# Kernel tuning notes

Hardware: AMD Instinct MI355X
Metric: run time of the kernel (lower is better)

## Reference

```python
import jax, jax.numpy as jnp
import numpy as np

B, T, E, H = 2, 1024, 1024, 16
HD = E // H
TEMP = 0.5


def setup_inputs() -> dict:
    key = jax.random.key(0)
    ks = jax.random.split(key, 20)
    d = {
        "query1": jax.random.normal(ks[0], (B, T, E), jnp.float32),
        "query2": jax.random.normal(ks[1], (B, T, E), jnp.float32),
        "key": jax.random.normal(ks[2], (B, T, E), jnp.float32),
        "value": jax.random.normal(ks[3], (B, T, E), jnp.float32),
    }
    s = 1.0 / np.sqrt(E)
    names = ["Wq", "Wq2", "Wq3", "Wk", "Wv", "Wo"]
    for i, n in enumerate(names):
        d[n] = jax.random.normal(ks[4 + i], (E, E), jnp.float32) * s
        d["b" + n[1:]] = jax.random.normal(ks[10 + i], (E,), jnp.float32) * 0.01
    return d


def _heads(x):
    # [B,T,E] -> [B,H,T,HD]
    b, t, _ = x.shape
    return x.reshape(b, t, H, HD).transpose(0, 2, 1, 3)


def reference(query1, query2, key, value,
              Wq, bq, Wq2, bq2, Wq3, bq3, Wk, bk, Wv, bv, Wo, bo):
    q = _heads(query1 @ Wq.T + bq)
    q2 = _heads(query2 @ Wq2.T + bq2)
    q3 = _heads(key @ Wq3.T + bq3)
    k = _heads(key @ Wk.T + bk)
    v = _heads(value @ Wv.T + bv)
    b, _, t, _ = q.shape
    scale = 1.0 / np.sqrt(HD)

    def global_attn(qx):
        s = jnp.einsum('bhtd,bhsd->bhts', qx, k) * scale  # [B,H,T,T]
        # global softmax over flattened T*T, temperature-scaled, times T
        a = jax.nn.softmax((s / TEMP).reshape(b, H, t * t), axis=-1)
        return a.reshape(b, H, t, t) * t

    a1 = global_attn(q)
    a2 = global_attn(q2)
    a3 = global_attn(q3)
    attn_out = jnp.einsum('bhts,bhsd->bthd', (a1 + a2 + a3) / 3.0, v)
    attn_out = attn_out.reshape(b, t, E)
    output = attn_out @ Wo.T + bo
    return output, a1
```

## Files before the change

kernel.cpp:

```cpp
#include <hip/hip_runtime.h>
#include <hip/hip_bf16.h>


#define B_ 2
#define T_ 1024
#define E_ 1024
#define H_ 16
#define HD_ 64
#define BH_ 32

typedef float f32x4 __attribute__((ext_vector_type(4)));
typedef short bfrag __attribute__((ext_vector_type(8)));

__device__ __forceinline__ unsigned short f2b(float f) {
  unsigned int u = __float_as_uint(f);
  u += 0x7fffu + ((u >> 16) & 1u);
  return (unsigned short)(u >> 16);
}

struct CvtArgs { const float* src[10]; unsigned short* dst[10]; int n[10]; };

__global__ __launch_bounds__(256) void cvt_kernel(CvtArgs a) {
  const int z = blockIdx.y;
  const float* __restrict__ s = a.src[z];
  unsigned short* __restrict__ d = a.dst[z];
  const int n = a.n[z];
  const int stride = gridDim.x * 256 * 4;
  for (int i = (blockIdx.x * 256 + threadIdx.x) * 4; i < n; i += stride) {
    float4 v = *(const float4*)(s + i);
    ushort4 o;
    o.x = f2b(v.x); o.y = f2b(v.y); o.z = f2b(v.z); o.w = f2b(v.w);
    *(ushort4*)(d + i) = o;
  }
}

__device__ __forceinline__ void mm128_core(const unsigned short* __restrict__ A,
                                           const unsigned short* __restrict__ W,
                                           int m0, int n0,
                                           unsigned short* As, unsigned short* Bs,
                                           f32x4 acc[4][4]) {
  const int tid  = threadIdx.x;
  const int lane = tid & 63, w = tid >> 6;
  const int lrow = lane & 15, quad = lane >> 4;
  const int wm = (w >> 1) * 64, wn = (w & 1) * 64;
  const int srow = tid >> 2, soff = (tid & 3) * 8;

  const unsigned short* Ar0 = A + (size_t)(m0 + srow) * E_ + soff;
  const unsigned short* Ar1 = Ar0 + (size_t)64 * E_;
  const unsigned short* Br0 = W + (size_t)(n0 + srow) * E_ + soff;
  const unsigned short* Br1 = Br0 + (size_t)64 * E_;

  for (int k0 = 0; k0 < E_; k0 += 32) {
    int4 a0 = *(const int4*)(Ar0 + k0);
    int4 a1 = *(const int4*)(Ar1 + k0);
    int4 b0 = *(const int4*)(Br0 + k0);
    int4 b1 = *(const int4*)(Br1 + k0);
    __syncthreads();
    *(int4*)(As + srow * 32 + soff)        = a0;
    *(int4*)(As + (srow + 64) * 32 + soff) = a1;
    *(int4*)(Bs + srow * 32 + soff)        = b0;
    *(int4*)(Bs + (srow + 64) * 32 + soff) = b1;
    __syncthreads();
    bfrag af[4], bf_[4];
#pragma unroll
    for (int mt = 0; mt < 4; mt++)
      af[mt] = *(const bfrag*)(As + (wm + mt * 16 + lrow) * 32 + quad * 8);
#pragma unroll
    for (int nt = 0; nt < 4; nt++)
      bf_[nt] = *(const bfrag*)(Bs + (wn + nt * 16 + lrow) * 32 + quad * 8);
#pragma unroll
    for (int mt = 0; mt < 4; mt++)
#pragma unroll
      for (int nt = 0; nt < 4; nt++)
        acc[mt][nt] = __builtin_amdgcn_mfma_f32_16x16x32_bf16(af[mt], bf_[nt], acc[mt][nt], 0, 0, 0);
  }
}

struct ProjArgs {
  const unsigned short* X[5];
  const unsigned short* W[5];
  const float* bias[5];
  unsigned short* dst[5];
};

__global__ __launch_bounds__(256) void proj_kernel(ProjArgs pa) {
  __shared__ unsigned short As[128 * 32];
  __shared__ unsigned short Bs[128 * 32];
  const int z = blockIdx.z;
  const int m0 = blockIdx.y * 128, n0 = blockIdx.x * 128;
  f32x4 acc[4][4];
#pragma unroll
  for (int mt = 0; mt < 4; mt++)
#pragma unroll
    for (int nt = 0; nt < 4; nt++) acc[mt][nt] = (f32x4)0.f;

  mm128_core(pa.X[z], pa.W[z], m0, n0, As, Bs, acc);

  const int tid = threadIdx.x, lane = tid & 63, w = tid >> 6;
  const int lrow = lane & 15, quad = lane >> 4;
  const int wm = (w >> 1) * 64, wn = (w & 1) * 64;
  const float* __restrict__ bias = pa.bias[z];
  unsigned short* __restrict__ dst = pa.dst[z];
  float bv[4];
#pragma unroll
  for (int nt = 0; nt < 4; nt++) bv[nt] = bias[n0 + wn + nt * 16 + lrow];
#pragma unroll
  for (int mt = 0; mt < 4; mt++)
#pragma unroll
    for (int nt = 0; nt < 4; nt++)
#pragma unroll
      for (int ii = 0; ii < 4; ii++) {
        const int m = m0 + wm + mt * 16 + quad * 4 + ii;
        const int n = n0 + wn + nt * 16 + lrow;
        const float v = acc[mt][nt][ii] + bv[nt];
        const int b = m >> 10, t = m & 1023, h = n >> 6, dd = n & 63;
        size_t idx;
        if (z == 4)
          idx = ((size_t)((b * H_ + h) * HD_ + dd)) * T_ + t;
        else
          idx = ((size_t)((b * H_ + h) * T_ + t)) * HD_ + dd;
        dst[idx] = f2b(v);
      }
}

__global__ __launch_bounds__(256) void attn_sums_kernel(
    const unsigned short* __restrict__ Q1, const unsigned short* __restrict__ Q2,
    const unsigned short* __restrict__ Q3, const unsigned short* __restrict__ Kh,
    float* __restrict__ sums) {
  const int tid = threadIdx.x, lane = tid & 63, w = tid >> 6;
  const int lrow = lane & 15, quad = lane >> 4;
  const int tw = w >> 1, sw = w & 1;
  const int bh = blockIdx.y;
  const int tb = blockIdx.x * 128 + tw * 64;
  const size_t base = (size_t)bh * T_ * HD_;
  const unsigned short* Qs[3] = {Q1 + base, Q2 + base, Q3 + base};
  const unsigned short* Kb = Kh + base;

  float lsum[3] = {0.f, 0.f, 0.f};
  for (int s0 = 0; s0 < T_; s0 += 128) {
    const int sb = s0 + sw * 64;
#pragma unroll
    for (int i = 0; i < 3; i++) {
      f32x4 acc[4][4];
#pragma unroll
      for (int mt = 0; mt < 4; mt++)
#pragma unroll
        for (int nt = 0; nt < 4; nt++) acc[mt][nt] = (f32x4)0.f;
#pragma unroll
      for (int kk = 0; kk < 2; kk++) {
        bfrag af[4], bf_[4];
#pragma unroll
        for (int mt = 0; mt < 4; mt++)
          af[mt] = *(const bfrag*)(Qs[i] + (size_t)(tb + mt * 16 + lrow) * HD_ + kk * 32 + quad * 8);
#pragma unroll
        for (int nt = 0; nt < 4; nt++)
          bf_[nt] = *(const bfrag*)(Kb + (size_t)(sb + nt * 16 + lrow) * HD_ + kk * 32 + quad * 8);
#pragma unroll
        for (int mt = 0; mt < 4; mt++)
#pragma unroll
          for (int nt = 0; nt < 4; nt++)
            acc[mt][nt] = __builtin_amdgcn_mfma_f32_16x16x32_bf16(af[mt], bf_[nt], acc[mt][nt], 0, 0, 0);
      }
      float s = 0.f;
#pragma unroll
      for (int mt = 0; mt < 4; mt++)
#pragma unroll
        for (int nt = 0; nt < 4; nt++)
#pragma unroll
          for (int ii = 0; ii < 4; ii++)
            s += __expf(acc[mt][nt][ii] * 0.25f);
      lsum[i] += s;
    }
  }
#pragma unroll
  for (int i = 0; i < 3; i++) {
    float v = lsum[i];
    for (int off = 32; off > 0; off >>= 1) v += __shfl_down(v, off, 64);
    if (lane == 0) atomicAdd(&sums[i * BH_ + bh], v);
  }
}

__global__ __launch_bounds__(256) void attn_main_kernel(
    const unsigned short* __restrict__ Q1, const unsigned short* __restrict__ Q2,
    const unsigned short* __restrict__ Q3, const unsigned short* __restrict__ Kh,
    const unsigned short* __restrict__ Vt, const float* __restrict__ sums,
    float* __restrict__ a1out, unsigned short* __restrict__ attn_out) {
  __shared__ unsigned short P[128 * 136];
  const int tid = threadIdx.x, lane = tid & 63, w = tid >> 6;
  const int lrow = lane & 15, quad = lane >> 4;
  const int tw = w >> 1, sw = w & 1, dw = sw;
  const int bh = blockIdx.y;
  const int b = bh >> 4, h = bh & 15;
  const int tb = blockIdx.x * 128 + tw * 64;
  const size_t base = (size_t)bh * T_ * HD_;
  const unsigned short* Qs[3] = {Q1 + base, Q2 + base, Q3 + base};
  const unsigned short* Kb = Kh + base;
  const unsigned short* Vb = Vt + (size_t)bh * HD_ * T_;

  float r[3];
#pragma unroll
  for (int i = 0; i < 3; i++) r[i] = (float)T_ / (3.f * sums[i * BH_ + bh]);
  const float a1s = 3.f * r[0];

  f32x4 oacc[4][2];
#pragma unroll
  for (int mt = 0; mt < 4; mt++) { oacc[mt][0] = (f32x4)0.f; oacc[mt][1] = (f32x4)0.f; }

  for (int s0 = 0; s0 < T_; s0 += 128) {
    const int sb = s0 + sw * 64;
    f32x4 pc[4][4];
#pragma unroll
    for (int mt = 0; mt < 4; mt++)
#pragma unroll
      for (int nt = 0; nt < 4; nt++) pc[mt][nt] = (f32x4)0.f;

#pragma unroll
    for (int i = 0; i < 3; i++) {
      f32x4 acc[4][4];
#pragma unroll
      for (int mt = 0; mt < 4; mt++)
#pragma unroll
        for (int nt = 0; nt < 4; nt++) acc[mt][nt] = (f32x4)0.f;
#pragma unroll
      for (int kk = 0; kk < 2; kk++) {
        bfrag af[4], bf_[4];
#pragma unroll
        for (int mt = 0; mt < 4; mt++)
          af[mt] = *(const bfrag*)(Qs[i] + (size_t)(tb + mt * 16 + lrow) * HD_ + kk * 32 + quad * 8);
#pragma unroll
        for (int nt = 0; nt < 4; nt++)
          bf_[nt] = *(const bfrag*)(Kb + (size_t)(sb + nt * 16 + lrow) * HD_ + kk * 32 + quad * 8);
#pragma unroll
        for (int mt = 0; mt < 4; mt++)
#pragma unroll
          for (int nt = 0; nt < 4; nt++)
            acc[mt][nt] = __builtin_amdgcn_mfma_f32_16x16x32_bf16(af[mt], bf_[nt], acc[mt][nt], 0, 0, 0);
      }
      const float ri = r[i];
#pragma unroll
      for (int mt = 0; mt < 4; mt++)
#pragma unroll
        for (int nt = 0; nt < 4; nt++)
#pragma unroll
          for (int ii = 0; ii < 4; ii++) {
            const float e = __expf(acc[mt][nt][ii] * 0.25f);
            pc[mt][nt][ii] += ri * e;
            if (i == 0) {
              const int t = tb + mt * 16 + quad * 4 + ii;
              const int s = sb + nt * 16 + lrow;
              a1out[((size_t)bh * T_ + t) * T_ + s] = e * a1s;
            }
          }
    }
    __syncthreads();
#pragma unroll
    for (int mt = 0; mt < 4; mt++)
#pragma unroll
      for (int nt = 0; nt < 4; nt++)
#pragma unroll
        for (int ii = 0; ii < 4; ii++) {
          const int tl = tw * 64 + mt * 16 + quad * 4 + ii;
          const int sl = sw * 64 + nt * 16 + lrow;
          P[tl * 136 + sl] = f2b(pc[mt][nt][ii]);
        }
    __syncthreads();
#pragma unroll
    for (int kk = 0; kk < 4; kk++) {
      bfrag pf[4], vf[2];
#pragma unroll
      for (int mt = 0; mt < 4; mt++)
        pf[mt] = *(const bfrag*)(P + (tw * 64 + mt * 16 + lrow) * 136 + kk * 32 + quad * 8);
#pragma unroll
      for (int nt = 0; nt < 2; nt++)
        vf[nt] = *(const bfrag*)(Vb + (size_t)(dw * 32 + nt * 16 + lrow) * T_ + s0 + kk * 32 + quad * 8);
#pragma unroll
      for (int mt = 0; mt < 4; mt++)
#pragma unroll
        for (int nt = 0; nt < 2; nt++)
          oacc[mt][nt] = __builtin_amdgcn_mfma_f32_16x16x32_bf16(pf[mt], vf[nt], oacc[mt][nt], 0, 0, 0);
    }
  }
#pragma unroll
  for (int mt = 0; mt < 4; mt++)
#pragma unroll
    for (int nt = 0; nt < 2; nt++)
#pragma unroll
      for (int ii = 0; ii < 4; ii++) {
        const int t = tb + mt * 16 + quad * 4 + ii;
        const int dd = dw * 32 + nt * 16 + lrow;
        attn_out[((size_t)(b * T_ + t)) * E_ + h * HD_ + dd] = f2b(oacc[mt][nt][ii]);
      }
}

__global__ __launch_bounds__(256) void outproj_kernel(
    const unsigned short* __restrict__ Ab, const unsigned short* __restrict__ Wb,
    const float* __restrict__ bias, float* __restrict__ out) {
  __shared__ unsigned short As[128 * 32];
  __shared__ unsigned short Bs[128 * 32];
  const int m0 = blockIdx.y * 128, n0 = blockIdx.x * 128;
  f32x4 acc[4][4];
#pragma unroll
  for (int mt = 0; mt < 4; mt++)
#pragma unroll
    for (int nt = 0; nt < 4; nt++) acc[mt][nt] = (f32x4)0.f;

  mm128_core(Ab, Wb, m0, n0, As, Bs, acc);

  const int tid = threadIdx.x, lane = tid & 63, w = tid >> 6;
  const int lrow = lane & 15, quad = lane >> 4;
  const int wm = (w >> 1) * 64, wn = (w & 1) * 64;
  float bv[4];
#pragma unroll
  for (int nt = 0; nt < 4; nt++) bv[nt] = bias[n0 + wn + nt * 16 + lrow];
#pragma unroll
  for (int mt = 0; mt < 4; mt++)
#pragma unroll
    for (int nt = 0; nt < 4; nt++)
#pragma unroll
      for (int ii = 0; ii < 4; ii++) {
        const int m = m0 + wm + mt * 16 + quad * 4 + ii;
        const int n = n0 + wn + nt * 16 + lrow;
        out[(size_t)m * E_ + n] = acc[mt][nt][ii] + bv[nt];
      }
}

extern "C" void kernel_launch(void* const* d_in, const int* in_sizes, int n_in,
                              void* d_out, int out_size, void* d_ws, size_t ws_size,
                              hipStream_t stream) {
  const float* q1f  = (const float*)d_in[0];
  const float* q2f  = (const float*)d_in[1];
  const float* keyf = (const float*)d_in[2];
  const float* valf = (const float*)d_in[3];
  const float* Wq  = (const float*)d_in[4];  const float* bq  = (const float*)d_in[5];
  const float* Wq2 = (const float*)d_in[6];  const float* bq2 = (const float*)d_in[7];
  const float* Wq3 = (const float*)d_in[8];  const float* bq3 = (const float*)d_in[9];
  const float* Wk  = (const float*)d_in[10]; const float* bk  = (const float*)d_in[11];
  const float* Wv  = (const float*)d_in[12]; const float* bv  = (const float*)d_in[13];
  const float* Wo  = (const float*)d_in[14]; const float* bo  = (const float*)d_in[15];

  char* ws = (char*)d_ws;
  const size_t MB = 1024 * 1024;
  unsigned short* xq1  = (unsigned short*)(ws + 0 * MB);
  unsigned short* xq2  = (unsigned short*)(ws + 4 * MB);
  unsigned short* xkey = (unsigned short*)(ws + 8 * MB);
  unsigned short* xval = (unsigned short*)(ws + 12 * MB);
  unsigned short* wq   = (unsigned short*)(ws + 16 * MB);
  unsigned short* wq2  = (unsigned short*)(ws + 18 * MB);
  unsigned short* wq3  = (unsigned short*)(ws + 20 * MB);
  unsigned short* wk   = (unsigned short*)(ws + 22 * MB);
  unsigned short* wv   = (unsigned short*)(ws + 24 * MB);
  unsigned short* wo   = (unsigned short*)(ws + 26 * MB);
  unsigned short* Qh1  = (unsigned short*)(ws + 28 * MB);
  unsigned short* Qh2  = (unsigned short*)(ws + 32 * MB);
  unsigned short* Qh3  = (unsigned short*)(ws + 36 * MB);
  unsigned short* Kh   = (unsigned short*)(ws + 40 * MB);
  unsigned short* Vt   = (unsigned short*)(ws + 44 * MB);
  unsigned short* attn = (unsigned short*)(ws + 48 * MB);
  float* sums          = (float*)(ws + 52 * MB);

  CvtArgs ca;
  const float* srcs[10] = {q1f, q2f, keyf, valf, Wq, Wq2, Wq3, Wk, Wv, Wo};
  unsigned short* dsts[10] = {xq1, xq2, xkey, xval, wq, wq2, wq3, wk, wv, wo};
  for (int i = 0; i < 10; i++) { ca.src[i] = srcs[i]; ca.dst[i] = dsts[i]; ca.n[i] = (i < 4) ? 2097152 : 1048576; }
  cvt_kernel<<<dim3(2048, 10), 256, 0, stream>>>(ca);

  hipMemsetAsync(sums, 0, 3 * BH_ * sizeof(float), stream);

  ProjArgs pa;
  const unsigned short* Xs[5] = {xq1, xq2, xkey, xkey, xval};
  const unsigned short* Ws_[5] = {wq, wq2, wq3, wk, wv};
  const float* Bi[5] = {bq, bq2, bq3, bk, bv};
  unsigned short* Ds[5] = {Qh1, Qh2, Qh3, Kh, Vt};
  for (int i = 0; i < 5; i++) { pa.X[i] = Xs[i]; pa.W[i] = Ws_[i]; pa.bias[i] = Bi[i]; pa.dst[i] = Ds[i]; }
  proj_kernel<<<dim3(8, 16, 5), 256, 0, stream>>>(pa);

  attn_sums_kernel<<<dim3(8, BH_), 256, 0, stream>>>(Qh1, Qh2, Qh3, Kh, sums);

  float* out = (float*)d_out;
  attn_main_kernel<<<dim3(8, BH_), 256, 0, stream>>>(Qh1, Qh2, Qh3, Kh, Vt, sums,
                                                     out + 2097152, attn);

  outproj_kernel<<<dim3(8, 16), 256, 0, stream>>>(attn, wo, bo, out);
}
```

Before: 372.1 us.

## Shrink attention tiles for more blocks, use exp2 and direct global-to-LDS loads

```diff
diff --git a/kernel.cpp b/kernel.cpp
--- a/kernel.cpp
+++ b/kernel.cpp
@@ -9,6 +9,8 @@
 #define HD_ 64
 #define BH_ 32
 
+#define CEXP 0.36067376022224085f
+
 typedef float f32x4 __attribute__((ext_vector_type(4)));
 typedef short bfrag __attribute__((ext_vector_type(8)));
 
@@ -16,6 +18,15 @@
   unsigned int u = __float_as_uint(f);
   u += 0x7fffu + ((u >> 16) & 1u);
   return (unsigned short)(u >> 16);
+}
+
+__device__ __forceinline__ void gl_lds16(const unsigned short* g, unsigned short* l) {
+  __builtin_amdgcn_global_load_lds(
+      reinterpret_cast<const __attribute__((address_space(1))) unsigned int*>(
+          reinterpret_cast<uintptr_t>(g)),
+      reinterpret_cast<__attribute__((address_space(3))) unsigned int*>(
+          reinterpret_cast<uintptr_t>(l)),
+      16, 0, 0);
 }
 
 struct CvtArgs { const float* src[10]; unsigned short* dst[10]; int n[10]; };
@@ -49,17 +60,17 @@
   const unsigned short* Ar1 = Ar0 + (size_t)64 * E_;
   const unsigned short* Br0 = W + (size_t)(n0 + srow) * E_ + soff;
   const unsigned short* Br1 = Br0 + (size_t)64 * E_;
+  unsigned short* Ad0 = As + tid * 8;
+  unsigned short* Ad1 = As + 2048 + tid * 8;
+  unsigned short* Bd0 = Bs + tid * 8;
+  unsigned short* Bd1 = Bs + 2048 + tid * 8;
 
   for (int k0 = 0; k0 < E_; k0 += 32) {
-    int4 a0 = *(const int4*)(Ar0 + k0);
-    int4 a1 = *(const int4*)(Ar1 + k0);
-    int4 b0 = *(const int4*)(Br0 + k0);
-    int4 b1 = *(const int4*)(Br1 + k0);
     __syncthreads();
-    *(int4*)(As + srow * 32 + soff)        = a0;
-    *(int4*)(As + (srow + 64) * 32 + soff) = a1;
-    *(int4*)(Bs + srow * 32 + soff)        = b0;
-    *(int4*)(Bs + (srow + 64) * 32 + soff) = b1;
+    gl_lds16(Ar0 + k0, Ad0);
+    gl_lds16(Ar1 + k0, Ad1);
+    gl_lds16(Br0 + k0, Bd0);
+    gl_lds16(Br1 + k0, Bd1);
     __syncthreads();
     bfrag af[4], bf_[4];
 #pragma unroll
@@ -123,75 +134,79 @@
       }
 }
 
-__global__ __launch_bounds__(256) void attn_sums_kernel(
+__global__ __launch_bounds__(256, 4) void attn_sums_kernel(
     const unsigned short* __restrict__ Q1, const unsigned short* __restrict__ Q2,
     const unsigned short* __restrict__ Q3, const unsigned short* __restrict__ Kh,
     float* __restrict__ sums) {
   const int tid = threadIdx.x, lane = tid & 63, w = tid >> 6;
   const int lrow = lane & 15, quad = lane >> 4;
   const int tw = w >> 1, sw = w & 1;
-  const int bh = blockIdx.y;
-  const int tb = blockIdx.x * 128 + tw * 64;
+  const int bh = blockIdx.z;
+  const int tb = blockIdx.x * 64 + tw * 32;
+  const int sbase = blockIdx.y * 512;
   const size_t base = (size_t)bh * T_ * HD_;
   const unsigned short* Qs[3] = {Q1 + base, Q2 + base, Q3 + base};
   const unsigned short* Kb = Kh + base;
 
-  float lsum[3] = {0.f, 0.f, 0.f};
-  for (int s0 = 0; s0 < T_; s0 += 128) {
-    const int sb = s0 + sw * 64;
+  float ls[3][4];
+#pragma unroll
+  for (int i = 0; i < 3; i++)
+#pragma unroll
+    for (int ii = 0; ii < 4; ii++) ls[i][ii] = 0.f;
+
+  for (int j = 0; j < 4; j++) {
+    const int sb = sbase + j * 128 + sw * 64;
 #pragma unroll
     for (int i = 0; i < 3; i++) {
-      f32x4 acc[4][4];
-#pragma unroll
-      for (int mt = 0; mt < 4; mt++)
+      f32x4 acc[2][4];
+#pragma unroll
+      for (int mt = 0; mt < 2; mt++)
 #pragma unroll
         for (int nt = 0; nt < 4; nt++) acc[mt][nt] = (f32x4)0.f;
 #pragma unroll
       for (int kk = 0; kk < 2; kk++) {
-        bfrag af[4], bf_[4];
-#pragma unroll
-        for (int mt = 0; mt < 4; mt++)
+        bfrag af[2], bf_[4];
+#pragma unroll
+        for (int mt = 0; mt < 2; mt++)
           af[mt] = *(const bfrag*)(Qs[i] + (size_t)(tb + mt * 16 + lrow) * HD_ + kk * 32 + quad * 8);
 #pragma unroll
         for (int nt = 0; nt < 4; nt++)
           bf_[nt] = *(const bfrag*)(Kb + (size_t)(sb + nt * 16 + lrow) * HD_ + kk * 32 + quad * 8);
 #pragma unroll
-        for (int mt = 0; mt < 4; mt++)
+        for (int mt = 0; mt < 2; mt++)
 #pragma unroll
           for (int nt = 0; nt < 4; nt++)
             acc[mt][nt] = __builtin_amdgcn_mfma_f32_16x16x32_bf16(af[mt], bf_[nt], acc[mt][nt], 0, 0, 0);
       }
-      float s = 0.f;
-#pragma unroll
-      for (int mt = 0; mt < 4; mt++)
+#pragma unroll
+      for (int mt = 0; mt < 2; mt++)
 #pragma unroll
         for (int nt = 0; nt < 4; nt++)
 #pragma unroll
           for (int ii = 0; ii < 4; ii++)
-            s += __expf(acc[mt][nt][ii] * 0.25f);
-      lsum[i] += s;
+            ls[i][ii] += exp2f(acc[mt][nt][ii] * CEXP);
     }
   }
 #pragma unroll
   for (int i = 0; i < 3; i++) {
-    float v = lsum[i];
+    float v = (ls[i][0] + ls[i][1]) + (ls[i][2] + ls[i][3]);
     for (int off = 32; off > 0; off >>= 1) v += __shfl_down(v, off, 64);
     if (lane == 0) atomicAdd(&sums[i * BH_ + bh], v);
   }
 }
 
-__global__ __launch_bounds__(256) void attn_main_kernel(
+__global__ __launch_bounds__(256, 2) void attn_main_kernel(
     const unsigned short* __restrict__ Q1, const unsigned short* __restrict__ Q2,
     const unsigned short* __restrict__ Q3, const unsigned short* __restrict__ Kh,
     const unsigned short* __restrict__ Vt, const float* __restrict__ sums,
     float* __restrict__ a1out, unsigned short* __restrict__ attn_out) {
-  __shared__ unsigned short P[128 * 136];
+  __shared__ unsigned short P[64 * 136];
   const int tid = threadIdx.x, lane = tid & 63, w = tid >> 6;
   const int lrow = lane & 15, quad = lane >> 4;
   const int tw = w >> 1, sw = w & 1, dw = sw;
   const int bh = blockIdx.y;
   const int b = bh >> 4, h = bh & 15;
-  const int tb = blockIdx.x * 128 + tw * 64;
+  const int tb = blockIdx.x * 64 + tw * 32;
   const size_t base = (size_t)bh * T_ * HD_;
   const unsigned short* Qs[3] = {Q1 + base, Q2 + base, Q3 + base};
   const unsigned short* Kb = Kh + base;
@@ -202,48 +217,48 @@
   for (int i = 0; i < 3; i++) r[i] = (float)T_ / (3.f * sums[i * BH_ + bh]);
   const float a1s = 3.f * r[0];
 
-  f32x4 oacc[4][2];
-#pragma unroll
-  for (int mt = 0; mt < 4; mt++) { oacc[mt][0] = (f32x4)0.f; oacc[mt][1] = (f32x4)0.f; }
+  f32x4 oacc[2][2];
+#pragma unroll
+  for (int mt = 0; mt < 2; mt++) { oacc[mt][0] = (f32x4)0.f; oacc[mt][1] = (f32x4)0.f; }
 
   for (int s0 = 0; s0 < T_; s0 += 128) {
     const int sb = s0 + sw * 64;
-    f32x4 pc[4][4];
-#pragma unroll
-    for (int mt = 0; mt < 4; mt++)
+    f32x4 pc[2][4];
+#pragma unroll
+    for (int mt = 0; mt < 2; mt++)
 #pragma unroll
       for (int nt = 0; nt < 4; nt++) pc[mt][nt] = (f32x4)0.f;
 
 #pragma unroll
     for (int i = 0; i < 3; i++) {
-      f32x4 acc[4][4];
-#pragma unroll
-      for (int mt = 0; mt < 4; mt++)
+      f32x4 acc[2][4];
+#pragma unroll
+      for (int mt = 0; mt < 2; mt++)
 #pragma unroll
         for (int nt = 0; nt < 4; nt++) acc[mt][nt] = (f32x4)0.f;
 #pragma unroll
       for (int kk = 0; kk < 2; kk++) {
-        bfrag af[4], bf_[4];
-#pragma unroll
-        for (int mt = 0; mt < 4; mt++)
+        bfrag af[2], bf_[4];
+#pragma unroll
+        for (int mt = 0; mt < 2; mt++)
           af[mt] = *(const bfrag*)(Qs[i] + (size_t)(tb + mt * 16 + lrow) * HD_ + kk * 32 + quad * 8);
 #pragma unroll
         for (int nt = 0; nt < 4; nt++)
           bf_[nt] = *(const bfrag*)(Kb + (size_t)(sb + nt * 16 + lrow) * HD_ + kk * 32 + quad * 8);
 #pragma unroll
-        for (int mt = 0; mt < 4; mt++)
+        for (int mt = 0; mt < 2; mt++)
 #pragma unroll
           for (int nt = 0; nt < 4; nt++)
             acc[mt][nt] = __builtin_amdgcn_mfma_f32_16x16x32_bf16(af[mt], bf_[nt], acc[mt][nt], 0, 0, 0);
       }
       const float ri = r[i];
 #pragma unroll
-      for (int mt = 0; mt < 4; mt++)
+      for (int mt = 0; mt < 2; mt++)
 #pragma unroll
         for (int nt = 0; nt < 4; nt++)
 #pragma unroll
           for (int ii = 0; ii < 4; ii++) {
-            const float e = __expf(acc[mt][nt][ii] * 0.25f);
+            const float e = exp2f(acc[mt][nt][ii] * CEXP);
             pc[mt][nt][ii] += ri * e;
             if (i == 0) {
               const int t = tb + mt * 16 + quad * 4 + ii;
@@ -254,34 +269,34 @@
     }
     __syncthreads();
 #pragma unroll
-    for (int mt = 0; mt < 4; mt++)
+    for (int mt = 0; mt < 2; mt++)
 #pragma unroll
       for (int nt = 0; nt < 4; nt++)
 #pragma unroll
         for (int ii = 0; ii < 4; ii++) {
-          const int tl = tw * 64 + mt * 16 + quad * 4 + ii;
+          const int tl = tw * 32 + mt * 16 + quad * 4 + ii;
           const int sl = sw * 64 + nt * 16 + lrow;
           P[tl * 136 + sl] = f2b(pc[mt][nt][ii]);
         }
     __syncthreads();
 #pragma unroll
     for (int kk = 0; kk < 4; kk++) {
-      bfrag pf[4], vf[2];
-#pragma unroll
-      for (int mt = 0; mt < 4; mt++)
-        pf[mt] = *(const bfrag*)(P + (tw * 64 + mt * 16 + lrow) * 136 + kk * 32 + quad * 8);
+      bfrag pf[2], vf[2];
+#pragma unroll
+      for (int mt = 0; mt < 2; mt++)
+        pf[mt] = *(const bfrag*)(P + (tw * 32 + mt * 16 + lrow) * 136 + kk * 32 + quad * 8);
 #pragma unroll
       for (int nt = 0; nt < 2; nt++)
         vf[nt] = *(const bfrag*)(Vb + (size_t)(dw * 32 + nt * 16 + lrow) * T_ + s0 + kk * 32 + quad * 8);
 #pragma unroll
-      for (int mt = 0; mt < 4; mt++)
+      for (int mt = 0; mt < 2; mt++)
 #pragma unroll
         for (int nt = 0; nt < 2; nt++)
           oacc[mt][nt] = __builtin_amdgcn_mfma_f32_16x16x32_bf16(pf[mt], vf[nt], oacc[mt][nt], 0, 0, 0);
     }
   }
 #pragma unroll
-  for (int mt = 0; mt < 4; mt++)
+  for (int mt = 0; mt < 2; mt++)
 #pragma unroll
     for (int nt = 0; nt < 2; nt++)
 #pragma unroll
@@ -374,11 +389,11 @@
   for (int i = 0; i < 5; i++) { pa.X[i] = Xs[i]; pa.W[i] = Ws_[i]; pa.bias[i] = Bi[i]; pa.dst[i] = Ds[i]; }
   proj_kernel<<<dim3(8, 16, 5), 256, 0, stream>>>(pa);
 
-  attn_sums_kernel<<<dim3(8, BH_), 256, 0, stream>>>(Qh1, Qh2, Qh3, Kh, sums);
+  attn_sums_kernel<<<dim3(16, 2, BH_), 256, 0, stream>>>(Qh1, Qh2, Qh3, Kh, sums);
 
   float* out = (float*)d_out;
-  attn_main_kernel<<<dim3(8, BH_), 256, 0, stream>>>(Qh1, Qh2, Qh3, Kh, Vt, sums,
-                                                     out + 2097152, attn);
+  attn_main_kernel<<<dim3(16, BH_), 256, 0, stream>>>(Qh1, Qh2, Qh3, Kh, Vt, sums,
+                                                      out + 2097152, attn);
 
   outproj_kernel<<<dim3(8, 16), 256, 0, stream>>>(attn, wo, bo, out);
 }
```

Result: slower. 399.4 us (+7.3%).
